# Kernel tuning notes

Measured on AMD Instinct MI355X. Metric: run time of the kernel, lower is better.

## Reference

```python
import jax, jax.numpy as jnp
import numpy as np
import math

L, D, H, FF = 6, 512, 8, 2048
B, S = 8, 1024
EPS = 1e-5


def sin_pos_embedding(num_embeddings, dim, padding_idx=0):
    half = dim // 2
    freq = jnp.exp(jnp.arange(half, dtype=jnp.float32) * (-math.log(10000.0) / (half - 1)))
    ang = jnp.arange(num_embeddings, dtype=jnp.float32)[:, None] * freq[None, :]
    emb = jnp.concatenate([jnp.sin(ang), jnp.cos(ang)], axis=1)
    return emb.at[padding_idx].set(0.0)


def layer_norm(x, g, b):
    mu = jnp.mean(x, axis=-1, keepdims=True)
    var = jnp.mean(jnp.square(x - mu), axis=-1, keepdims=True)
    return (x - mu) * jax.lax.rsqrt(var + EPS) * g + b


def setup_inputs() -> dict:
    key = jax.random.key(0)
    ks = jax.random.split(key, 16)
    s = 0.02
    inp = {
        'x': jax.random.normal(ks[0], (B, S, D), jnp.float32),
        'char_ids': jax.random.randint(ks[1], (B, S), 0, 10000, jnp.int64) if jax.config.read('jax_enable_x64') else jax.random.randint(ks[1], (B, S), 0, 10000, jnp.int32),
        'seq_len': jnp.full((B,), S, jnp.int32),
        'mask': jnp.ones((B, S), jnp.int32),
        'Wqkv': jax.random.normal(ks[2], (L, D, 3 * D), jnp.float32) * s,
        'Wfc': jax.random.normal(ks[3], (L, D, D), jnp.float32) * s,
        'bfc': jnp.zeros((L, D), jnp.float32),
        'ln1_g': jnp.ones((L, D), jnp.float32), 'ln1_b': jnp.zeros((L, D), jnp.float32),
        'ln2_g': jnp.ones((L, D), jnp.float32), 'ln2_b': jnp.zeros((L, D), jnp.float32),
        'W1': jax.random.normal(ks[4], (L, D, FF), jnp.float32) * s,
        'b1': jnp.zeros((L, FF), jnp.float32),
        'W2': jax.random.normal(ks[5], (L, FF, D), jnp.float32) * s,
        'b2': jnp.zeros((L, D), jnp.float32),
    }
    return inp


def reference(x, char_ids, seq_len, mask, Wqkv, Wfc, bfc, ln1_g, ln1_b, ln2_g, ln2_b, W1, b1, W2, b2):
    # sinusoidal positional embedding computed from mask positions (padding_idx=0)
    valid = (mask != 0).astype(jnp.int32)
    positions = jnp.cumsum(valid, axis=1) * valid  # [B,S], pads -> 0
    table = sin_pos_embedding(S + 2, D)  # max_pos = padding_idx+1+S
    x = x + table[positions]

    key_mask = (mask == 0)[:, None, None, :]  # [B,1,1,S]
    dh = D // H

    for l in range(L):
        residual = x
        qkv = jnp.einsum('bsd,de->bse', x, Wqkv[l])  # [B,S,3D]
        q, k, v = jnp.split(qkv, 3, axis=-1)
        q = q.reshape(B, S, H, dh).transpose(0, 2, 1, 3)  # [B,H,S,dh]
        k = k.reshape(B, S, H, dh).transpose(0, 2, 1, 3)
        v = v.reshape(B, S, H, dh).transpose(0, 2, 1, 3)
        attn = jnp.einsum('bhqd,bhkd->bhqk', q, k)  # scale=1 (scale=False)
        attn = jnp.where(key_mask, -jnp.inf, attn)
        attn = jax.nn.softmax(attn, axis=-1)
        o = jnp.einsum('bhqk,bhkd->bhqd', attn, v)
        o = o.transpose(0, 2, 1, 3).reshape(B, S, D)
        o = jnp.einsum('bsd,de->bse', o, Wfc[l]) + bfc[l]
        x = layer_norm(o + residual, ln1_g[l], ln1_b[l])
        residual = x
        h = jax.nn.relu(jnp.einsum('bsd,df->bsf', x, W1[l]) + b1[l])
        h = jnp.einsum('bsf,fd->bsd', h, W2[l]) + b2[l]
        x = layer_norm(residual + h, ln2_g[l], ln2_b[l])
    return x
```

## Files before the change

kernel.cpp:

```cpp
#include <hip/hip_runtime.h>
#include <math.h>

#define LAYERS 6
#define DMODEL 512
#define NHEAD 8
#define DHEAD 64
#define FFDIM 2048
#define BATCH 8
#define SEQ 1024
#define ROWS (BATCH * SEQ)
#define EPS 1e-5f

typedef __attribute__((ext_vector_type(8))) short bf16x8;
typedef __attribute__((ext_vector_type(4))) float f32x4;

__device__ inline short f2bf(float f) {
    union { float f; unsigned u; } v; v.f = f;
    return (short)((v.u + 0x8000u) >> 16);
}
__device__ inline float bf2f(short s) {
    union { unsigned u; float f; } v;
    v.u = ((unsigned)(unsigned short)s) << 16;
    return v.f;
}

#define GLOAD_LDS16(g, l)                                                      \
    __builtin_amdgcn_global_load_lds(                                          \
        (__attribute__((address_space(1))) void*)(g),                          \
        (__attribute__((address_space(3))) void*)(l), 16, 0, 0)

__global__ void wtrans_kernel(const float* __restrict__ src, short* __restrict__ dst,
                              int K, int N) {
    __shared__ float t[32][33];
    const size_t mofs = (size_t)blockIdx.z * K * N;
    src += mofs; dst += mofs;
    int n0 = blockIdx.x * 32, k0 = blockIdx.y * 32;
    int tx = threadIdx.x, ty = threadIdx.y;
#pragma unroll
    for (int i = 0; i < 4; ++i)
        t[ty + 8 * i][tx] = src[(size_t)(k0 + ty + 8 * i) * N + n0 + tx];
    __syncthreads();
#pragma unroll
    for (int i = 0; i < 4; ++i)
        dst[(size_t)(n0 + ty + 8 * i) * K + k0 + tx] = f2bf(t[tx][ty + 8 * i]);
}

__global__ void pos_scan_kernel(const int* __restrict__ mask, int* __restrict__ pos) {
    __shared__ int sm[SEQ];
    int b = blockIdx.x;
    int t = threadIdx.x;
    int v = (mask[b * SEQ + t] != 0) ? 1 : 0;
    sm[t] = v;
    __syncthreads();
    for (int off = 1; off < SEQ; off <<= 1) {
        int add = (t >= off) ? sm[t - off] : 0;
        __syncthreads();
        sm[t] += add;
        __syncthreads();
    }
    pos[b * SEQ + t] = sm[t] * v;
}

__global__ void add_pos_kernel(const float* __restrict__ xin, const int* __restrict__ pos,
                               float* __restrict__ xout, short* __restrict__ xb) {
    int bs = blockIdx.x;
    int t = threadIdx.x;
    int p = pos[bs];
    int d0 = t * 4;
    const float C = -logf(10000.0f) * (1.0f / 255.0f);
    float4 xv = *(const float4*)(xin + (size_t)bs * DMODEL + d0);
    float e[4];
#pragma unroll
    for (int j = 0; j < 4; ++j) {
        int d = d0 + j;
        if (p == 0) {
            e[j] = 0.0f;
        } else {
            int dd = (d < 256) ? d : d - 256;
            float freq = expf((float)dd * C);
            float ang = (float)p * freq;
            e[j] = (d < 256) ? sinf(ang) : cosf(ang);
        }
    }
    float4 ov;
    ov.x = xv.x + e[0]; ov.y = xv.y + e[1]; ov.z = xv.z + e[2]; ov.w = xv.w + e[3];
    *(float4*)(xout + (size_t)bs * DMODEL + d0) = ov;
    short4 sb;
    sb.x = f2bf(ov.x); sb.y = f2bf(ov.y); sb.z = f2bf(ov.z); sb.w = f2bf(ov.w);
    *(short4*)(xb + (size_t)bs * DMODEL + d0) = sb;
}


template <bool OUTBF16, bool BIAS, bool RELU>
__global__ __launch_bounds__(256) void gemm_bf16_kernel(const short* __restrict__ A,
                                                        const short* __restrict__ BT,
                                                        const float* __restrict__ bias,
                                                        void* __restrict__ Cv,
                                                        int M, int N, int K) {
    __shared__ __attribute__((aligned(16))) short Asm[2][128 * 32];
    __shared__ __attribute__((aligned(16))) short Bsm[2][128 * 32];
    const int tid = threadIdx.x;
    const int w = tid >> 6;
    const int lane = tid & 63;
    const int quad = lane >> 4;
    const int lr = lane & 15;
    const int m0 = blockIdx.y * 128;
    const int n0 = blockIdx.x * 128;
    const int wm = (w >> 1) * 64;
    const int wn = (w & 1) * 64;

    const int segr = lane >> 2;
    const int segk = (((lane & 3) - (lane >> 3)) & 3) * 8;
    const int sA0 = w * 2, sA1 = w * 2 + 1;
    const short* gA0 = A + (size_t)(m0 + sA0 * 16 + segr) * K + segk;
    const short* gA1 = A + (size_t)(m0 + sA1 * 16 + segr) * K + segk;
    const short* gB0 = BT + (size_t)(n0 + sA0 * 16 + segr) * K + segk;
    const short* gB1 = BT + (size_t)(n0 + sA1 * 16 + segr) * K + segk;
    const int lofs0 = sA0 * 512 + lane * 8;
    const int lofs1 = sA1 * 512 + lane * 8;
    const int gp = ((quad + (lr >> 1)) & 3) * 8;

    f32x4 acc[4][4];
#pragma unroll
    for (int i = 0; i < 4; ++i)
#pragma unroll
        for (int j = 0; j < 4; ++j) { acc[i][j][0] = 0.f; acc[i][j][1] = 0.f; acc[i][j][2] = 0.f; acc[i][j][3] = 0.f; }

    GLOAD_LDS16(gA0, &Asm[0][lofs0]);
    GLOAD_LDS16(gA1, &Asm[0][lofs1]);
    GLOAD_LDS16(gB0, &Bsm[0][lofs0]);
    GLOAD_LDS16(gB1, &Bsm[0][lofs1]);

    const int nk = K >> 5;
    for (int i = 0; i < nk; ++i) {
        __syncthreads();
        if (i + 1 < nk) {
            const int k1 = (i + 1) * 32;
            const int nb = (i + 1) & 1;
            GLOAD_LDS16(gA0 + k1, &Asm[nb][lofs0]);
            GLOAD_LDS16(gA1 + k1, &Asm[nb][lofs1]);
            GLOAD_LDS16(gB0 + k1, &Bsm[nb][lofs0]);
            GLOAD_LDS16(gB1 + k1, &Bsm[nb][lofs1]);
        }
        const int cur = i & 1;
        bf16x8 af[4], bfr[4];
#pragma unroll
        for (int mt = 0; mt < 4; ++mt)
            af[mt] = *(const bf16x8*)&Asm[cur][(wm + mt * 16 + lr) * 32 + gp];
#pragma unroll
        for (int nt = 0; nt < 4; ++nt)
            bfr[nt] = *(const bf16x8*)&Bsm[cur][(wn + nt * 16 + lr) * 32 + gp];
#pragma unroll
        for (int mt = 0; mt < 4; ++mt)
#pragma unroll
            for (int nt = 0; nt < 4; ++nt)
                acc[mt][nt] = __builtin_amdgcn_mfma_f32_16x16x32_bf16(af[mt], bfr[nt], acc[mt][nt], 0, 0, 0);
    }

    float bv[4];
    if (BIAS) {
#pragma unroll
        for (int nt = 0; nt < 4; ++nt) bv[nt] = bias[n0 + wn + nt * 16 + lr];
    }
#pragma unroll
    for (int mt = 0; mt < 4; ++mt)
#pragma unroll
        for (int nt = 0; nt < 4; ++nt)
#pragma unroll
            for (int r = 0; r < 4; ++r) {
                float v = acc[mt][nt][r];
                if (BIAS) v += bv[nt];
                if (RELU) v = fmaxf(v, 0.f);
                int row = m0 + wm + mt * 16 + quad * 4 + r;
                int col = n0 + wn + nt * 16 + lr;
                if (OUTBF16)
                    ((short*)Cv)[(size_t)row * N + col] = f2bf(v);
                else
                    ((float*)Cv)[(size_t)row * N + col] = v;
            }
}

__global__ __launch_bounds__(256) void gemm_qkv_kernel(const short* __restrict__ A,
                                                       const short* __restrict__ BT,
                                                       short* __restrict__ qkv3,
                                                       int M, int N, int K) {
    __shared__ __attribute__((aligned(16))) short Asm[2][128 * 32];
    __shared__ __attribute__((aligned(16))) short Bsm[2][128 * 32];
    const int tid = threadIdx.x;
    const int w = tid >> 6;
    const int lane = tid & 63;
    const int quad = lane >> 4;
    const int lr = lane & 15;
    const int m0 = blockIdx.y * 128;
    const int n0 = blockIdx.x * 128;
    const int wm = (w >> 1) * 64;
    const int wn = (w & 1) * 64;

    const int segr = lane >> 2;
    const int segk = (((lane & 3) - (lane >> 3)) & 3) * 8;
    const int sA0 = w * 2, sA1 = w * 2 + 1;
    const short* gA0 = A + (size_t)(m0 + sA0 * 16 + segr) * K + segk;
    const short* gA1 = A + (size_t)(m0 + sA1 * 16 + segr) * K + segk;
    const short* gB0 = BT + (size_t)(n0 + sA0 * 16 + segr) * K + segk;
    const short* gB1 = BT + (size_t)(n0 + sA1 * 16 + segr) * K + segk;
    const int lofs0 = sA0 * 512 + lane * 8;
    const int lofs1 = sA1 * 512 + lane * 8;
    const int gp = ((quad + (lr >> 1)) & 3) * 8;

    f32x4 acc[4][4];
#pragma unroll
    for (int i = 0; i < 4; ++i)
#pragma unroll
        for (int j = 0; j < 4; ++j) { acc[i][j][0] = 0.f; acc[i][j][1] = 0.f; acc[i][j][2] = 0.f; acc[i][j][3] = 0.f; }

    GLOAD_LDS16(gA0, &Asm[0][lofs0]);
    GLOAD_LDS16(gA1, &Asm[0][lofs1]);
    GLOAD_LDS16(gB0, &Bsm[0][lofs0]);
    GLOAD_LDS16(gB1, &Bsm[0][lofs1]);

    const int nk = K >> 5;
    for (int i = 0; i < nk; ++i) {
        __syncthreads();
        if (i + 1 < nk) {
            const int k1 = (i + 1) * 32;
            const int nb = (i + 1) & 1;
            GLOAD_LDS16(gA0 + k1, &Asm[nb][lofs0]);
            GLOAD_LDS16(gA1 + k1, &Asm[nb][lofs1]);
            GLOAD_LDS16(gB0 + k1, &Bsm[nb][lofs0]);
            GLOAD_LDS16(gB1 + k1, &Bsm[nb][lofs1]);
        }
        const int cur = i & 1;
        bf16x8 af[4], bfr[4];
#pragma unroll
        for (int mt = 0; mt < 4; ++mt)
            af[mt] = *(const bf16x8*)&Asm[cur][(wm + mt * 16 + lr) * 32 + gp];
#pragma unroll
        for (int nt = 0; nt < 4; ++nt)
            bfr[nt] = *(const bf16x8*)&Bsm[cur][(wn + nt * 16 + lr) * 32 + gp];
#pragma unroll
        for (int mt = 0; mt < 4; ++mt)
#pragma unroll
            for (int nt = 0; nt < 4; ++nt)
                acc[mt][nt] = __builtin_amdgcn_mfma_f32_16x16x32_bf16(af[mt], bfr[nt], acc[mt][nt], 0, 0, 0);
    }

#pragma unroll
    for (int nt = 0; nt < 4; ++nt) {
        const int col = n0 + wn + nt * 16 + lr;
        const int which = col >> 9;
        const int h = (col >> 6) & 7;
        const int d = col & 63;
#pragma unroll
        for (int mt = 0; mt < 4; ++mt)
#pragma unroll
            for (int r = 0; r < 4; ++r) {
                int row = m0 + wm + mt * 16 + quad * 4 + r;
                int bb = row >> 10, s = row & 1023;
                qkv3[((size_t)(which * 64 + bb * 8 + h) * SEQ + s) * DHEAD + d] =
                    f2bf(acc[mt][nt][r]);
            }
    }
}

__global__ __launch_bounds__(256) void gemm_ks_kernel(const short* __restrict__ A,
                                                      const short* __restrict__ BT,
                                                      short* __restrict__ Cp,
                                                      int M, int N, int Kfull, int Khalf) {
    __shared__ __attribute__((aligned(16))) short Asm[2][64 * 32];
    __shared__ __attribute__((aligned(16))) short Bsm[2][128 * 32];
    const int tid = threadIdx.x;
    const int w = tid >> 6;
    const int lane = tid & 63;
    const int quad = lane >> 4;
    const int lr = lane & 15;
    const int m0 = blockIdx.y * 64;
    const int n0 = blockIdx.x * 128;
    const int kofs = blockIdx.z * Khalf;
    short* C = Cp + (size_t)blockIdx.z * M * N;
    const int wm = (w >> 1) * 32;
    const int wn = (w & 1) * 64;

    const int segr = lane >> 2;
    const int segk = (((lane & 3) - (lane >> 3)) & 3) * 8;
    const short* gA  = A + (size_t)(m0 + w * 16 + segr) * Kfull + kofs + segk;
    const short* gB0 = BT + (size_t)(n0 + (2 * w) * 16 + segr) * Kfull + kofs + segk;
    const short* gB1 = BT + (size_t)(n0 + (2 * w + 1) * 16 + segr) * Kfull + kofs + segk;
    const int lA  = w * 512 + lane * 8;
    const int lB0 = (2 * w) * 512 + lane * 8;
    const int lB1 = (2 * w + 1) * 512 + lane * 8;
    const int gp = ((quad + (lr >> 1)) & 3) * 8;

    f32x4 acc[2][4];
#pragma unroll
    for (int i = 0; i < 2; ++i)
#pragma unroll
        for (int j = 0; j < 4; ++j) { acc[i][j][0] = 0.f; acc[i][j][1] = 0.f; acc[i][j][2] = 0.f; acc[i][j][3] = 0.f; }

    GLOAD_LDS16(gA, &Asm[0][lA]);
    GLOAD_LDS16(gB0, &Bsm[0][lB0]);
    GLOAD_LDS16(gB1, &Bsm[0][lB1]);

    const int nk = Khalf >> 5;
    for (int i = 0; i < nk; ++i) {
        __syncthreads();
        if (i + 1 < nk) {
            const int k1 = (i + 1) * 32;
            const int nb = (i + 1) & 1;
            GLOAD_LDS16(gA + k1, &Asm[nb][lA]);
            GLOAD_LDS16(gB0 + k1, &Bsm[nb][lB0]);
            GLOAD_LDS16(gB1 + k1, &Bsm[nb][lB1]);
        }
        const int cur = i & 1;
        bf16x8 af[2], bfr[4];
#pragma unroll
        for (int mt = 0; mt < 2; ++mt)
            af[mt] = *(const bf16x8*)&Asm[cur][(wm + mt * 16 + lr) * 32 + gp];
#pragma unroll
        for (int nt = 0; nt < 4; ++nt)
            bfr[nt] = *(const bf16x8*)&Bsm[cur][(wn + nt * 16 + lr) * 32 + gp];
#pragma unroll
        for (int mt = 0; mt < 2; ++mt)
#pragma unroll
            for (int nt = 0; nt < 4; ++nt)
                acc[mt][nt] = __builtin_amdgcn_mfma_f32_16x16x32_bf16(af[mt], bfr[nt], acc[mt][nt], 0, 0, 0);
    }

#pragma unroll
    for (int mt = 0; mt < 2; ++mt)
#pragma unroll
        for (int nt = 0; nt < 4; ++nt)
#pragma unroll
            for (int r = 0; r < 4; ++r) {
                int row = m0 + wm + mt * 16 + quad * 4 + r;
                int col = n0 + wn + nt * 16 + lr;
                C[(size_t)row * N + col] = f2bf(acc[mt][nt][r]);
            }
}

#define QTILE 64
__global__ __launch_bounds__(256) void attn_mfma_kernel(const short* __restrict__ qhm,
                                                        const short* __restrict__ khm,
                                                        const short* __restrict__ vhm,
                                                        const int* __restrict__ mask,
                                                        short* __restrict__ o) {
    __shared__ __attribute__((aligned(16))) short Ks[2][64 * 64];
    __shared__ __attribute__((aligned(16))) short Vt[2][64][72];
    __shared__ __attribute__((aligned(16))) short Ps[4][16][72];
    __shared__ float Msf[2][64];

    const int bx = blockIdx.x;
    const int qt = bx >> 6;
    const int bh = bx & 63;
    const int b = bh >> 3, h = bh & 7;
    const int tid = threadIdx.x;
    const int w = tid >> 6;
    const int lane = tid & 63;
    const int quad = lane >> 4;
    const int lr = lane & 15;
    const size_t hbase = (size_t)bh * SEQ * DHEAD;
    const size_t seqrow = (size_t)b * SEQ;

    bf16x8 qf[2];
#pragma unroll
    for (int c = 0; c < 2; ++c)
        qf[c] = *(const bf16x8*)(qhm + hbase +
            (size_t)(qt * QTILE + w * 16 + lr) * DHEAD + c * 32 + quad * 8);

    const int krow0 = w * 16 + (lane >> 3);
    const int kg0 = (((lane & 7) - (lane >> 4)) & 7) * 8;
    const int kg1 = (((lane & 7) - 4 - (lane >> 4)) & 7) * 8;
    const short* gK0 = khm + hbase + (size_t)krow0 * DHEAD + kg0;
    const short* gK1 = khm + hbase + (size_t)(krow0 + 8) * DHEAD + kg1;
    const int lK0 = w * 16 * 64 + lane * 8;
    const int lK1 = (w * 16 + 8) * 64 + lane * 8;
    const int kp0 = ((quad + (lr >> 1)) & 7) * 8;
    const int kp1 = ((4 + quad + (lr >> 1)) & 7) * 8;

    const int vkp = tid & 31;
    const int vdg = tid >> 5;
    const short* gV = vhm + hbase + (size_t)(2 * vkp) * DHEAD + vdg * 8;

    bf16x8 r0, r1;
    int mreg = 0;

    GLOAD_LDS16(gK0, &Ks[0][lK0]);
    GLOAD_LDS16(gK1, &Ks[0][lK1]);
    {
        r0 = *(const bf16x8*)(gV);
        r1 = *(const bf16x8*)(gV + DHEAD);
#pragma unroll
        for (int i = 0; i < 8; ++i) {
            short2 p; p.x = r0[i]; p.y = r1[i];
            *(short2*)&Vt[0][vdg * 8 + i][vkp * 2] = p;
        }
        if (tid < 64) Msf[0][tid] = mask[seqrow + tid] ? 1.0f : 0.0f;
    }
    __syncthreads();

    f32x4 Oacc[4];
    float rs[4];
#pragma unroll
    for (int t2 = 0; t2 < 4; ++t2) { Oacc[t2][0] = 0.f; Oacc[t2][1] = 0.f; Oacc[t2][2] = 0.f; Oacc[t2][3] = 0.f; }
#pragma unroll
    for (int r = 0; r < 4; ++r) rs[r] = 0.f;

    for (int kt = 0; kt < 16; ++kt) {
        const int cur = kt & 1;
        const int nb = cur ^ 1;
        const int ktn = (kt + 1) & 15;
        GLOAD_LDS16(gK0 + (size_t)ktn * 64 * DHEAD, &Ks[nb][lK0]);
        GLOAD_LDS16(gK1 + (size_t)ktn * 64 * DHEAD, &Ks[nb][lK1]);
        {
            const size_t ofs = (size_t)ktn * 64 * DHEAD;
            r0 = *(const bf16x8*)(gV + ofs);
            r1 = *(const bf16x8*)(gV + ofs + DHEAD);
            if (tid < 64) mreg = mask[seqrow + ktn * 64 + tid];
        }
        bf16x8 kf[2][4], vf[2][4];
#pragma unroll
        for (int t = 0; t < 4; ++t) {
            kf[0][t] = *(const bf16x8*)&Ks[cur][(lr + 16 * t) * 64 + kp0];
            kf[1][t] = *(const bf16x8*)&Ks[cur][(lr + 16 * t) * 64 + kp1];
            vf[0][t] = *(const bf16x8*)&Vt[cur][lr + 16 * t][quad * 8];
            vf[1][t] = *(const bf16x8*)&Vt[cur][lr + 16 * t][quad * 8 + 32];
        }
        float mv[4];
#pragma unroll
        for (int t = 0; t < 4; ++t) mv[t] = Msf[cur][lr + 16 * t];

        f32x4 S[4];
#pragma unroll
        for (int t = 0; t < 4; ++t) { S[t][0] = 0.f; S[t][1] = 0.f; S[t][2] = 0.f; S[t][3] = 0.f; }
#pragma unroll
        for (int c = 0; c < 2; ++c)
#pragma unroll
            for (int t = 0; t < 4; ++t)
                S[t] = __builtin_amdgcn_mfma_f32_16x16x32_bf16(qf[c], kf[c][t], S[t], 0, 0, 0);
#pragma unroll
        for (int t = 0; t < 4; ++t)
#pragma unroll
            for (int r = 0; r < 4; ++r) {
                float p = __expf(S[t][r] - 8.0f) * mv[t];
                S[t][r] = p;
                rs[r] += p;
            }
#pragma unroll
        for (int t = 0; t < 4; ++t)
#pragma unroll
            for (int r = 0; r < 4; ++r)
                Ps[w][quad * 4 + r][lr + 16 * t] = f2bf(S[t][r]);
        bf16x8 pa0 = *(const bf16x8*)&Ps[w][lr][quad * 8];
        bf16x8 pa1 = *(const bf16x8*)&Ps[w][lr][quad * 8 + 32];
#pragma unroll
        for (int t2 = 0; t2 < 4; ++t2) {
            Oacc[t2] = __builtin_amdgcn_mfma_f32_16x16x32_bf16(pa0, vf[0][t2], Oacc[t2], 0, 0, 0);
            Oacc[t2] = __builtin_amdgcn_mfma_f32_16x16x32_bf16(pa1, vf[1][t2], Oacc[t2], 0, 0, 0);
        }
        {
#pragma unroll
            for (int i = 0; i < 8; ++i) {
                short2 p; p.x = r0[i]; p.y = r1[i];
                *(short2*)&Vt[nb][vdg * 8 + i][vkp * 2] = p;
            }
            if (tid < 64) Msf[nb][tid] = mreg ? 1.0f : 0.0f;
        }
        __syncthreads();
    }

    float inv[4];
#pragma unroll
    for (int r = 0; r < 4; ++r) {
        float v = rs[r];
        v += __shfl_xor(v, 1);
        v += __shfl_xor(v, 2);
        v += __shfl_xor(v, 4);
        v += __shfl_xor(v, 8);
        inv[r] = 1.f / v;
    }
#pragma unroll
    for (int t2 = 0; t2 < 4; ++t2)
#pragma unroll
        for (int r = 0; r < 4; ++r) {
            int row = qt * QTILE + w * 16 + quad * 4 + r;
            o[(seqrow + row) * DMODEL + h * DHEAD + 16 * t2 + lr] = f2bf(Oacc[t2][r] * inv[r]);
        }
}

__global__ __launch_bounds__(64) void ln3_kernel(const short* __restrict__ t0,
                                                 const short* __restrict__ t1,
                                                 const float* __restrict__ bias,
                                                 float* __restrict__ x,
                                                 short* __restrict__ xb,
                                                 const float* __restrict__ g,
                                                 const float* __restrict__ bta) {
    const int row = blockIdx.x;
    const int t = threadIdx.x;
    const size_t base = (size_t)row * DMODEL + t * 8;
    float4 x0 = *(const float4*)(x + base);
    float4 x1 = *(const float4*)(x + base + 4);
    bf16x8 a0 = *(const bf16x8*)(t0 + base);
    bf16x8 a1 = *(const bf16x8*)(t1 + base);
    float4 bi0 = *(const float4*)(bias + t * 8);
    float4 bi1 = *(const float4*)(bias + t * 8 + 4);
    float v[8];
    v[0] = x0.x + bf2f(a0[0]) + bf2f(a1[0]) + bi0.x;
    v[1] = x0.y + bf2f(a0[1]) + bf2f(a1[1]) + bi0.y;
    v[2] = x0.z + bf2f(a0[2]) + bf2f(a1[2]) + bi0.z;
    v[3] = x0.w + bf2f(a0[3]) + bf2f(a1[3]) + bi0.w;
    v[4] = x1.x + bf2f(a0[4]) + bf2f(a1[4]) + bi1.x;
    v[5] = x1.y + bf2f(a0[5]) + bf2f(a1[5]) + bi1.y;
    v[6] = x1.z + bf2f(a0[6]) + bf2f(a1[6]) + bi1.z;
    v[7] = x1.w + bf2f(a0[7]) + bf2f(a1[7]) + bi1.w;
    float s = 0.f, sq = 0.f;
#pragma unroll
    for (int i = 0; i < 8; ++i) { s += v[i]; sq += v[i] * v[i]; }
#pragma unroll
    for (int off = 1; off < 64; off <<= 1) {
        s += __shfl_xor(s, off);
        sq += __shfl_xor(sq, off);
    }
    float mu = s * (1.0f / DMODEL);
    float var = sq * (1.0f / DMODEL) - mu * mu;
    float r = rsqrtf(var + EPS);
    float4 g0 = *(const float4*)(g + t * 8);
    float4 g1 = *(const float4*)(g + t * 8 + 4);
    float4 b0 = *(const float4*)(bta + t * 8);
    float4 b1 = *(const float4*)(bta + t * 8 + 4);
    float ov[8];
    ov[0] = (v[0] - mu) * r * g0.x + b0.x;
    ov[1] = (v[1] - mu) * r * g0.y + b0.y;
    ov[2] = (v[2] - mu) * r * g0.z + b0.z;
    ov[3] = (v[3] - mu) * r * g0.w + b0.w;
    ov[4] = (v[4] - mu) * r * g1.x + b1.x;
    ov[5] = (v[5] - mu) * r * g1.y + b1.y;
    ov[6] = (v[6] - mu) * r * g1.z + b1.z;
    ov[7] = (v[7] - mu) * r * g1.w + b1.w;
    *(float4*)(x + base) = *(float4*)&ov[0];
    *(float4*)(x + base + 4) = *(float4*)&ov[4];
    bf16x8 ob;
#pragma unroll
    for (int i = 0; i < 8; ++i) ob[i] = f2bf(ov[i]);
    *(bf16x8*)(xb + base) = ob;
}

extern "C" void kernel_launch(void* const* d_in, const int* in_sizes, int n_in,
                              void* d_out, int out_size, void* d_ws, size_t ws_size,
                              hipStream_t stream) {
    const float* x_in  = (const float*)d_in[0];
    const int*   mask  = (const int*)d_in[3];
    const float* Wqkv  = (const float*)d_in[4];
    const float* Wfc   = (const float*)d_in[5];
    const float* bfc   = (const float*)d_in[6];
    const float* ln1_g = (const float*)d_in[7];
    const float* ln1_b = (const float*)d_in[8];
    const float* ln2_g = (const float*)d_in[9];
    const float* ln2_b = (const float*)d_in[10];
    const float* W1    = (const float*)d_in[11];
    const float* b1    = (const float*)d_in[12];
    const float* W2    = (const float*)d_in[13];
    const float* b2    = (const float*)d_in[14];

    float* x = (float*)d_out;

    char* ws = (char*)d_ws;
    size_t ofs = 0;
    int*   pos   = (int*)ws;                 ofs += 65536;
    short* tmp0  = (short*)(ws + ofs);       ofs += (size_t)ROWS * DMODEL * 2;
    short* tmp1  = (short*)(ws + ofs);       ofs += (size_t)ROWS * DMODEL * 2;
    short* xb    = (short*)(ws + ofs);       ofs += (size_t)ROWS * DMODEL * 2;
    short* qkv3  = (short*)(ws + ofs);
    short* hb    = (short*)(ws + ofs);
    ofs += (size_t)ROWS * 3 * DMODEL * 2;
    short* obuf  = (short*)(ws + ofs);       ofs += (size_t)ROWS * DMODEL * 2;
    short* WqkvT = (short*)(ws + ofs);       ofs += (size_t)LAYERS * DMODEL * 3 * DMODEL * 2;
    short* WfcT  = (short*)(ws + ofs);       ofs += (size_t)LAYERS * DMODEL * DMODEL * 2;
    short* W1T   = (short*)(ws + ofs);       ofs += (size_t)LAYERS * DMODEL * FFDIM * 2;
    short* W2T   = (short*)(ws + ofs);       ofs += (size_t)LAYERS * FFDIM * DMODEL * 2;

    wtrans_kernel<<<dim3(3 * DMODEL / 32, DMODEL / 32, LAYERS), dim3(32, 8), 0, stream>>>(
        Wqkv, WqkvT, DMODEL, 3 * DMODEL);
    wtrans_kernel<<<dim3(DMODEL / 32, DMODEL / 32, LAYERS), dim3(32, 8), 0, stream>>>(
        Wfc, WfcT, DMODEL, DMODEL);
    wtrans_kernel<<<dim3(FFDIM / 32, DMODEL / 32, LAYERS), dim3(32, 8), 0, stream>>>(
        W1, W1T, DMODEL, FFDIM);
    wtrans_kernel<<<dim3(DMODEL / 32, FFDIM / 32, LAYERS), dim3(32, 8), 0, stream>>>(
        W2, W2T, FFDIM, DMODEL);

    pos_scan_kernel<<<BATCH, SEQ, 0, stream>>>(mask, pos);
    add_pos_kernel<<<ROWS, 128, 0, stream>>>(x_in, pos, x, xb);

    short* qhm = qkv3;
    short* khm = qkv3 + (size_t)64 * SEQ * DHEAD;
    short* vhm = qkv3 + (size_t)128 * SEQ * DHEAD;

    for (int l = 0; l < LAYERS; ++l) {
        const short* wqkvT_l = WqkvT + (size_t)l * DMODEL * 3 * DMODEL;
        const short* wfcT_l  = WfcT + (size_t)l * DMODEL * DMODEL;
        const short* w1T_l   = W1T + (size_t)l * DMODEL * FFDIM;
        const short* w2T_l   = W2T + (size_t)l * FFDIM * DMODEL;
        const float* bfc_l   = bfc + (size_t)l * DMODEL;
        const float* b1_l    = b1 + (size_t)l * FFDIM;
        const float* b2_l    = b2 + (size_t)l * DMODEL;

        gemm_qkv_kernel<<<dim3(3 * DMODEL / 128, ROWS / 128), 256, 0, stream>>>(
            xb, wqkvT_l, qkv3, ROWS, 3 * DMODEL, DMODEL);
        attn_mfma_kernel<<<1024, 256, 0, stream>>>(qhm, khm, vhm, mask, obuf);
        gemm_ks_kernel<<<dim3(DMODEL / 128, ROWS / 64, 2), 256, 0, stream>>>(
            obuf, wfcT_l, tmp0, ROWS, DMODEL, DMODEL, DMODEL / 2);
        ln3_kernel<<<ROWS, 64, 0, stream>>>(tmp0, tmp1, bfc_l, x, xb,
                                            ln1_g + (size_t)l * DMODEL,
                                            ln1_b + (size_t)l * DMODEL);
        gemm_bf16_kernel<true, true, true><<<dim3(FFDIM / 128, ROWS / 128), 256, 0, stream>>>(
            xb, w1T_l, b1_l, hb, ROWS, FFDIM, DMODEL);
        gemm_ks_kernel<<<dim3(DMODEL / 128, ROWS / 64, 2), 256, 0, stream>>>(
            hb, w2T_l, tmp0, ROWS, DMODEL, FFDIM, FFDIM / 2);
        ln3_kernel<<<ROWS, 64, 0, stream>>>(tmp0, tmp1, b2_l, x, xb,
                                            ln2_g + (size_t)l * DMODEL,
                                            ln2_b + (size_t)l * DMODEL);
    }
}
```

Measured before the change: 1.159 ms.

## Write V transposed from QKV GEMM and load K/V fragments directly to registers in attention

The QKV GEMM epilogue now stores V transposed per head (d-major), so attention can load V fragments straight from global memory without an LDS transpose. The attention kernel drops the K/V shared-memory staging and its barriers. It register-double-buffers K, V and mask fragments loaded directly from global, and doubles the query tile to 128 rows per block so each K/V load is reused across two M-tiles. The mask is precomputed as floats in the scan kernel. This trades LDS traffic and syncs for higher register pressure and redundant per-wave global loads that now rely on the cache.

```diff
diff --git a/kernel.cpp b/kernel.cpp
--- a/kernel.cpp
+++ b/kernel.cpp
@@ -45,12 +45,14 @@
         dst[(size_t)(n0 + ty + 8 * i) * K + k0 + tx] = f2bf(t[tx][ty + 8 * i]);
 }
 
-__global__ void pos_scan_kernel(const int* __restrict__ mask, int* __restrict__ pos) {
+__global__ void pos_scan_kernel(const int* __restrict__ mask, int* __restrict__ pos,
+                                float* __restrict__ maskf) {
     __shared__ int sm[SEQ];
     int b = blockIdx.x;
     int t = threadIdx.x;
     int v = (mask[b * SEQ + t] != 0) ? 1 : 0;
     sm[t] = v;
+    maskf[b * SEQ + t] = v ? 1.0f : 0.0f;
     __syncthreads();
     for (int off = 1; off < SEQ; off <<= 1) {
         int add = (t >= off) ? sm[t - off] : 0;
@@ -251,14 +253,23 @@
         const int h = (col >> 6) & 7;
         const int d = col & 63;
 #pragma unroll
-        for (int mt = 0; mt < 4; ++mt)
-#pragma unroll
-            for (int r = 0; r < 4; ++r) {
-                int row = m0 + wm + mt * 16 + quad * 4 + r;
-                int bb = row >> 10, s = row & 1023;
-                qkv3[((size_t)(which * 64 + bb * 8 + h) * SEQ + s) * DHEAD + d] =
-                    f2bf(acc[mt][nt][r]);
+        for (int mt = 0; mt < 4; ++mt) {
+            int row0 = m0 + wm + mt * 16 + quad * 4;
+            int bb = row0 >> 10, s0 = row0 & 1023;
+            if (which == 2) {
+                short4 pk;
+                pk.x = f2bf(acc[mt][nt][0]);
+                pk.y = f2bf(acc[mt][nt][1]);
+                pk.z = f2bf(acc[mt][nt][2]);
+                pk.w = f2bf(acc[mt][nt][3]);
+                *(short4*)&qkv3[((size_t)(128 + bb * 8 + h) * DHEAD + d) * SEQ + s0] = pk;
+            } else {
+#pragma unroll
+                for (int r = 0; r < 4; ++r)
+                    qkv3[((size_t)(which * 64 + bb * 8 + h) * SEQ + s0 + r) * DHEAD + d] =
+                        f2bf(acc[mt][nt][r]);
             }
+        }
     }
 }
 
@@ -337,16 +348,13 @@
             }
 }
 
-#define QTILE 64
-__global__ __launch_bounds__(256) void attn_mfma_kernel(const short* __restrict__ qhm,
-                                                        const short* __restrict__ khm,
-                                                        const short* __restrict__ vhm,
-                                                        const int* __restrict__ mask,
-                                                        short* __restrict__ o) {
-    __shared__ __attribute__((aligned(16))) short Ks[2][64 * 64];
-    __shared__ __attribute__((aligned(16))) short Vt[2][64][72];
+#define QTILE 128
+__global__ __launch_bounds__(256, 2) void attn_mfma_kernel(const short* __restrict__ qhm,
+                                                           const short* __restrict__ khm,
+                                                           const short* __restrict__ vhmT,
+                                                           const float* __restrict__ maskf,
+                                                           short* __restrict__ o) {
     __shared__ __attribute__((aligned(16))) short Ps[4][16][72];
-    __shared__ float Msf[2][64];
 
     const int bx = blockIdx.x;
     const int qt = bx >> 6;
@@ -357,133 +365,116 @@
     const int lane = tid & 63;
     const int quad = lane >> 4;
     const int lr = lane & 15;
-    const size_t hbase = (size_t)bh * SEQ * DHEAD;
     const size_t seqrow = (size_t)b * SEQ;
 
-    bf16x8 qf[2];
-#pragma unroll
-    for (int c = 0; c < 2; ++c)
-        qf[c] = *(const bf16x8*)(qhm + hbase +
-            (size_t)(qt * QTILE + w * 16 + lr) * DHEAD + c * 32 + quad * 8);
-
-    const int krow0 = w * 16 + (lane >> 3);
-    const int kg0 = (((lane & 7) - (lane >> 4)) & 7) * 8;
-    const int kg1 = (((lane & 7) - 4 - (lane >> 4)) & 7) * 8;
-    const short* gK0 = khm + hbase + (size_t)krow0 * DHEAD + kg0;
-    const short* gK1 = khm + hbase + (size_t)(krow0 + 8) * DHEAD + kg1;
-    const int lK0 = w * 16 * 64 + lane * 8;
-    const int lK1 = (w * 16 + 8) * 64 + lane * 8;
-    const int kp0 = ((quad + (lr >> 1)) & 7) * 8;
-    const int kp1 = ((4 + quad + (lr >> 1)) & 7) * 8;
-
-    const int vkp = tid & 31;
-    const int vdg = tid >> 5;
-    const short* gV = vhm + hbase + (size_t)(2 * vkp) * DHEAD + vdg * 8;
-
-    bf16x8 r0, r1;
-    int mreg = 0;
-
-    GLOAD_LDS16(gK0, &Ks[0][lK0]);
-    GLOAD_LDS16(gK1, &Ks[0][lK1]);
-    {
-        r0 = *(const bf16x8*)(gV);
-        r1 = *(const bf16x8*)(gV + DHEAD);
-#pragma unroll
-        for (int i = 0; i < 8; ++i) {
-            short2 p; p.x = r0[i]; p.y = r1[i];
-            *(short2*)&Vt[0][vdg * 8 + i][vkp * 2] = p;
+    const size_t qbase = (size_t)bh * SEQ * DHEAD;
+    bf16x8 qf[2][2];
+#pragma unroll
+    for (int mt = 0; mt < 2; ++mt)
+#pragma unroll
+        for (int c = 0; c < 2; ++c)
+            qf[mt][c] = *(const bf16x8*)(qhm + qbase +
+                (size_t)(qt * QTILE + w * 32 + mt * 16 + lr) * DHEAD + c * 32 + quad * 8);
+
+    const short* gKf = khm + qbase + (size_t)lr * DHEAD + quad * 8;
+    const short* gVf = vhmT + (size_t)bh * DHEAD * SEQ + (size_t)lr * SEQ + quad * 8;
+    const float* gM = maskf + seqrow + lr;
+
+    f32x4 Oacc[2][4];
+    float rs[2][4];
+#pragma unroll
+    for (int mt = 0; mt < 2; ++mt)
+#pragma unroll
+        for (int t2 = 0; t2 < 4; ++t2) { Oacc[mt][t2][0] = 0.f; Oacc[mt][t2][1] = 0.f; Oacc[mt][t2][2] = 0.f; Oacc[mt][t2][3] = 0.f; }
+#pragma unroll
+    for (int mt = 0; mt < 2; ++mt)
+#pragma unroll
+        for (int r = 0; r < 4; ++r) { rs[mt][r] = 0.f; }
+
+    bf16x8 kfA[2][4], vfA[2][4], kfB[2][4], vfB[2][4];
+    float mvA[4], mvB[4];
+
+#pragma unroll
+    for (int t = 0; t < 4; ++t) {
+        kfA[0][t] = *(const bf16x8*)(gKf + (size_t)(16 * t) * DHEAD);
+        kfA[1][t] = *(const bf16x8*)(gKf + (size_t)(16 * t) * DHEAD + 32);
+        vfA[0][t] = *(const bf16x8*)(gVf + (size_t)(16 * t) * SEQ);
+        vfA[1][t] = *(const bf16x8*)(gVf + (size_t)(16 * t) * SEQ + 32);
+        mvA[t] = gM[16 * t];
+    }
+
+#define ATTN_STEP(KF, VF, MV, KFN, VFN, MVN, KT)                               \
+    {                                                                          \
+        const int ktn = ((KT) + 1) & 15;                                       \
+        const size_t ko = (size_t)ktn * 64 * DHEAD;                            \
+        const size_t vo = (size_t)ktn * 64;                                    \
+        _Pragma("unroll")                                                      \
+        for (int t = 0; t < 4; ++t) {                                          \
+            KFN[0][t] = *(const bf16x8*)(gKf + ko + (size_t)(16 * t) * DHEAD); \
+            KFN[1][t] = *(const bf16x8*)(gKf + ko + (size_t)(16 * t) * DHEAD + 32); \
+            VFN[0][t] = *(const bf16x8*)(gVf + vo + (size_t)(16 * t) * SEQ);   \
+            VFN[1][t] = *(const bf16x8*)(gVf + vo + (size_t)(16 * t) * SEQ + 32); \
+            MVN[t] = gM[ktn * 64 + 16 * t];                                    \
+        }                                                                      \
+        _Pragma("unroll")                                                      \
+        for (int mt = 0; mt < 2; ++mt) {                                       \
+            f32x4 S[4];                                                        \
+            _Pragma("unroll")                                                  \
+            for (int t = 0; t < 4; ++t) { S[t][0] = 0.f; S[t][1] = 0.f; S[t][2] = 0.f; S[t][3] = 0.f; } \
+            _Pragma("unroll")                                                  \
+            for (int c = 0; c < 2; ++c)                                        \
+                _Pragma("unroll")                                              \
+                for (int t = 0; t < 4; ++t)                                    \
+                    S[t] = __builtin_amdgcn_mfma_f32_16x16x32_bf16(qf[mt][c], KF[c][t], S[t], 0, 0, 0); \
+            _Pragma("unroll")                                                  \
+            for (int t = 0; t < 4; ++t)                                        \
+                _Pragma("unroll")                                              \
+                for (int r = 0; r < 4; ++r) {                                  \
+                    float p = __expf(S[t][r] - 8.0f) * MV[t];                  \
+                    S[t][r] = p;                                               \
+                    rs[mt][r] += p;                                            \
+                }                                                              \
+            _Pragma("unroll")                                                  \
+            for (int t = 0; t < 4; ++t)                                        \
+                _Pragma("unroll")                                              \
+                for (int r = 0; r < 4; ++r)                                    \
+                    Ps[w][quad * 4 + r][lr + 16 * t] = f2bf(S[t][r]);          \
+            bf16x8 pa0 = *(const bf16x8*)&Ps[w][lr][quad * 8];                 \
+            bf16x8 pa1 = *(const bf16x8*)&Ps[w][lr][quad * 8 + 32];            \
+            _Pragma("unroll")                                                  \
+            for (int t2 = 0; t2 < 4; ++t2) {                                   \
+                Oacc[mt][t2] = __builtin_amdgcn_mfma_f32_16x16x32_bf16(pa0, VF[0][t2], Oacc[mt][t2], 0, 0, 0); \
+                Oacc[mt][t2] = __builtin_amdgcn_mfma_f32_16x16x32_bf16(pa1, VF[1][t2], Oacc[mt][t2], 0, 0, 0); \
+            }                                                                  \
+        }                                                                      \
+    }
+
+    for (int kt = 0; kt < 16; kt += 2) {
+        ATTN_STEP(kfA, vfA, mvA, kfB, vfB, mvB, kt);
+        ATTN_STEP(kfB, vfB, mvB, kfA, vfA, mvA, kt + 1);
+    }
+#undef ATTN_STEP
+
+#pragma unroll
+    for (int mt = 0; mt < 2; ++mt) {
+        float inv[4];
+#pragma unroll
+        for (int r = 0; r < 4; ++r) {
+            float v = rs[mt][r];
+            v += __shfl_xor(v, 1);
+            v += __shfl_xor(v, 2);
+            v += __shfl_xor(v, 4);
+            v += __shfl_xor(v, 8);
+            inv[r] = 1.f / v;
         }
-        if (tid < 64) Msf[0][tid] = mask[seqrow + tid] ? 1.0f : 0.0f;
-    }
-    __syncthreads();
-
-    f32x4 Oacc[4];
-    float rs[4];
-#pragma unroll
-    for (int t2 = 0; t2 < 4; ++t2) { Oacc[t2][0] = 0.f; Oacc[t2][1] = 0.f; Oacc[t2][2] = 0.f; Oacc[t2][3] = 0.f; }
-#pragma unroll
-    for (int r = 0; r < 4; ++r) rs[r] = 0.f;
-
-    for (int kt = 0; kt < 16; ++kt) {
-        const int cur = kt & 1;
-        const int nb = cur ^ 1;
-        const int ktn = (kt + 1) & 15;
-        GLOAD_LDS16(gK0 + (size_t)ktn * 64 * DHEAD, &Ks[nb][lK0]);
-        GLOAD_LDS16(gK1 + (size_t)ktn * 64 * DHEAD, &Ks[nb][lK1]);
-        {
-            const size_t ofs = (size_t)ktn * 64 * DHEAD;
-            r0 = *(const bf16x8*)(gV + ofs);
-            r1 = *(const bf16x8*)(gV + ofs + DHEAD);
-            if (tid < 64) mreg = mask[seqrow + ktn * 64 + tid];
-        }
-        bf16x8 kf[2][4], vf[2][4];
-#pragma unroll
-        for (int t = 0; t < 4; ++t) {
-            kf[0][t] = *(const bf16x8*)&Ks[cur][(lr + 16 * t) * 64 + kp0];
-            kf[1][t] = *(const bf16x8*)&Ks[cur][(lr + 16 * t) * 64 + kp1];
-            vf[0][t] = *(const bf16x8*)&Vt[cur][lr + 16 * t][quad * 8];
-            vf[1][t] = *(const bf16x8*)&Vt[cur][lr + 16 * t][quad * 8 + 32];
-        }
-        float mv[4];
-#pragma unroll
-        for (int t = 0; t < 4; ++t) mv[t] = Msf[cur][lr + 16 * t];
-
-        f32x4 S[4];
-#pragma unroll
-        for (int t = 0; t < 4; ++t) { S[t][0] = 0.f; S[t][1] = 0.f; S[t][2] = 0.f; S[t][3] = 0.f; }
-#pragma unroll
-        for (int c = 0; c < 2; ++c)
-#pragma unroll
-            for (int t = 0; t < 4; ++t)
-                S[t] = __builtin_amdgcn_mfma_f32_16x16x32_bf16(qf[c], kf[c][t], S[t], 0, 0, 0);
-#pragma unroll
-        for (int t = 0; t < 4; ++t)
+#pragma unroll
+        for (int t2 = 0; t2 < 4; ++t2)
 #pragma unroll
             for (int r = 0; r < 4; ++r) {
-                float p = __expf(S[t][r] - 8.0f) * mv[t];
-                S[t][r] = p;
-                rs[r] += p;
+                int row = qt * QTILE + w * 32 + mt * 16 + quad * 4 + r;
+                o[(seqrow + row) * DMODEL + h * DHEAD + 16 * t2 + lr] = f2bf(Oacc[mt][t2][r] * inv[r]);
             }
-#pragma unroll
-        for (int t = 0; t < 4; ++t)
-#pragma unroll
-            for (int r = 0; r < 4; ++r)
-                Ps[w][quad * 4 + r][lr + 16 * t] = f2bf(S[t][r]);
-        bf16x8 pa0 = *(const bf16x8*)&Ps[w][lr][quad * 8];
-        bf16x8 pa1 = *(const bf16x8*)&Ps[w][lr][quad * 8 + 32];
-#pragma unroll
-        for (int t2 = 0; t2 < 4; ++t2) {
-            Oacc[t2] = __builtin_amdgcn_mfma_f32_16x16x32_bf16(pa0, vf[0][t2], Oacc[t2], 0, 0, 0);
-            Oacc[t2] = __builtin_amdgcn_mfma_f32_16x16x32_bf16(pa1, vf[1][t2], Oacc[t2], 0, 0, 0);
-        }
-        {
-#pragma unroll
-            for (int i = 0; i < 8; ++i) {
-                short2 p; p.x = r0[i]; p.y = r1[i];
-                *(short2*)&Vt[nb][vdg * 8 + i][vkp * 2] = p;
-            }
-            if (tid < 64) Msf[nb][tid] = mreg ? 1.0f : 0.0f;
-        }
-        __syncthreads();
-    }
-
-    float inv[4];
-#pragma unroll
-    for (int r = 0; r < 4; ++r) {
-        float v = rs[r];
-        v += __shfl_xor(v, 1);
-        v += __shfl_xor(v, 2);
-        v += __shfl_xor(v, 4);
-        v += __shfl_xor(v, 8);
-        inv[r] = 1.f / v;
-    }
-#pragma unroll
-    for (int t2 = 0; t2 < 4; ++t2)
-#pragma unroll
-        for (int r = 0; r < 4; ++r) {
-            int row = qt * QTILE + w * 16 + quad * 4 + r;
-            o[(seqrow + row) * DMODEL + h * DHEAD + 16 * t2 + lr] = f2bf(Oacc[t2][r] * inv[r]);
-        }
+    }
 }
 
 __global__ __launch_bounds__(64) void ln3_kernel(const short* __restrict__ t0,
@@ -564,7 +555,8 @@
 
     char* ws = (char*)d_ws;
     size_t ofs = 0;
-    int*   pos   = (int*)ws;                 ofs += 65536;
+    int*   pos   = (int*)ws;
+    float* maskf = (float*)(ws + 32768);     ofs += 65536;
     short* tmp0  = (short*)(ws + ofs);       ofs += (size_t)ROWS * DMODEL * 2;
     short* tmp1  = (short*)(ws + ofs);       ofs += (size_t)ROWS * DMODEL * 2;
     short* xb    = (short*)(ws + ofs);       ofs += (size_t)ROWS * DMODEL * 2;
@@ -586,12 +578,12 @@
     wtrans_kernel<<<dim3(DMODEL / 32, FFDIM / 32, LAYERS), dim3(32, 8), 0, stream>>>(
         W2, W2T, FFDIM, DMODEL);
 
-    pos_scan_kernel<<<BATCH, SEQ, 0, stream>>>(mask, pos);
+    pos_scan_kernel<<<BATCH, SEQ, 0, stream>>>(mask, pos, maskf);
     add_pos_kernel<<<ROWS, 128, 0, stream>>>(x_in, pos, x, xb);
 
-    short* qhm = qkv3;
-    short* khm = qkv3 + (size_t)64 * SEQ * DHEAD;
-    short* vhm = qkv3 + (size_t)128 * SEQ * DHEAD;
+    short* qhm  = qkv3;
+    short* khm  = qkv3 + (size_t)64 * SEQ * DHEAD;
+    short* vhmT = qkv3 + (size_t)128 * SEQ * DHEAD;
 
     for (int l = 0; l < LAYERS; ++l) {
         const short* wqkvT_l = WqkvT + (size_t)l * DMODEL * 3 * DMODEL;
@@ -604,7 +596,7 @@
 
         gemm_qkv_kernel<<<dim3(3 * DMODEL / 128, ROWS / 128), 256, 0, stream>>>(
             xb, wqkvT_l, qkv3, ROWS, 3 * DMODEL, DMODEL);
-        attn_mfma_kernel<<<1024, 256, 0, stream>>>(qhm, khm, vhm, mask, obuf);
+        attn_mfma_kernel<<<512, 256, 0, stream>>>(qhm, khm, vhmT, maskf, obuf);
         gemm_ks_kernel<<<dim3(DMODEL / 128, ROWS / 64, 2), 256, 0, stream>>>(
             obuf, wfcT_l, tmp0, ROWS, DMODEL, DMODEL, DMODEL / 2);
         ln3_kernel<<<ROWS, 64, 0, stream>>>(tmp0, tmp1, bfc_l, x, xb,
```

New measurement: 1.282 ms. +10.6%, slower.
